# Optimization experiments

Hardware: AMD Instinct MI355X
Metric: run time of the kernel (lower is better)

Reference implementation:

```python
import jax, jax.numpy as jnp
import numpy as np

COEF_MEMORY = 0.2

def setup_inputs() -> dict:
    key = jax.random.key(0)
    k1, k2, k3, k4 = jax.random.split(key, 4)
    B, T, HW, C, Cv, M = 2, 8, 4096, 64, 3, 1024
    k = jax.random.normal(k1, (B, T, HW, C), dtype=jnp.float32)
    v = jax.random.normal(k2, (B, T, HW, Cv), dtype=jnp.float32)
    m_k = jax.random.normal(k3, (B, T - 1, M, C), dtype=jnp.float32)
    m_v = jax.random.normal(k4, (B, T - 1, M, Cv), dtype=jnp.float32)
    return {"k": k, "v": v, "m_k": m_k, "m_v": m_v}

def reference(k, v, m_k, m_v):
    # k: [B,T,HW,C] frame keys; v: [B,T,HW,Cv] frame values (quarter-res images)
    # m_k: [B,T-1,M,C] memory keys at step i; m_v: [B,T-1,M,Cv] memory values
    c = COEF_MEMORY
    k_i = k[:, :-1]  # ref keys  [B,T-1,HW,C]
    k_j = k[:, 1:]   # tar keys  [B,T-1,HW,C]
    v_i = v[:, :-1]  # ref vals  [B,T-1,HW,Cv]
    # frame-to-frame affinity: softmax over ref positions (last axis)
    sim_k = jax.nn.softmax(jnp.einsum('btqc,btkc->btqk', k_j, k_i), axis=-1)
    # memory-to-frame affinity: softmax over memory slots
    sim_m = jax.nn.softmax(jnp.einsum('btqc,btmc->btqm', k_j, m_k), axis=-1)
    rec_k = jnp.einsum('btqk,btkd->btqd', sim_k, v_i)   # [B,T-1,HW,Cv]
    rec_m = jnp.einsum('btqm,btmd->btqd', sim_m, m_v)   # [B,T-1,HW,Cv]
    return (1.0 - c) * rec_k + c * rec_m
```

## Files before the change

### kernel.cpp

```cpp
#include <hip/hip_runtime.h>

typedef __attribute__((ext_vector_type(2))) __fp16 h2;
typedef __attribute__((ext_vector_type(4))) __fp16 h4;
typedef __attribute__((ext_vector_type(8))) __fp16 h8;
typedef __attribute__((ext_vector_type(4))) float f32x4;

#define LOG2E 1.44269504088896340736f

__device__ __forceinline__ h2 pkrtz(float a, float b) {
    return __builtin_bit_cast(h2, __builtin_amdgcn_cvt_pkrtz(a, b));
}

__global__ __launch_bounds__(256) void kast_attn_kernel(
    const float* __restrict__ K,
    const float* __restrict__ V,
    const float* __restrict__ MK,
    const float* __restrict__ MV,
    float* __restrict__ OUT)
{
    __shared__ alignas(16) __fp16 sK[2][64][64];
    __shared__ alignas(16) __fp16 sVT[2][4][68];

    const int id = blockIdx.x;
    const int sw = (id & 7) * 112 + (id >> 3);
    const int bt = sw >> 6;
    const int qblk = sw & 63;
    const int b = bt / 7, t = bt % 7;

    const int tid = threadIdx.x;
    const int lane = tid & 63;
    const int w = tid >> 6;
    const int col = lane & 15;
    const int g = lane >> 4;

    const int r = tid >> 2;
    const int c0 = (tid & 3) * 16;
    const int rs = (r & 7) << 3;
    const unsigned vr = (unsigned)tid / 3u;
    const unsigned vd = (unsigned)tid - vr * 3u;

    if (tid < 128) sVT[tid >> 6][3][tid & 63] = (__fp16)1.0f;

    const float* Qbase = K + (((size_t)b * 8 + (t + 1)) * 4096) * 64;
    h8 aq[2];
    {
        const int qrow = qblk * 64 + w * 16 + col;
        const float* qp = Qbase + (size_t)qrow * 64;
#pragma unroll
        for (int ch = 0; ch < 2; ++ch) {
            const int cc = ch * 32 + g * 8;
            const f32x4 xa = *(const f32x4*)&qp[cc];
            const f32x4 xb = *(const f32x4*)&qp[cc + 4];
            const h2 p0 = pkrtz(xa[0] * LOG2E, xa[1] * LOG2E);
            const h2 p1 = pkrtz(xa[2] * LOG2E, xa[3] * LOG2E);
            const h2 p2 = pkrtz(xb[0] * LOG2E, xb[1] * LOG2E);
            const h2 p3 = pkrtz(xb[2] * LOG2E, xb[3] * LOG2E);
            aq[ch] = (h8){p0[0], p0[1], p1[0], p1[1], p2[0], p2[1], p3[0], p3[1]};
        }
    }

    float outc0 = 0.f, outc1 = 0.f, outc2 = 0.f;

    for (int phase = 0; phase < 2; ++phase) {
        const float* kp; const float* vp; int ntile; float wgt;
        if (phase == 0) {
            kp = K + (((size_t)b * 8 + t) * 4096) * 64;
            vp = V + (((size_t)b * 8 + t) * 4096) * 3;
            ntile = 64; wgt = 0.8f;
        } else {
            kp = MK + (((size_t)b * 7 + t) * 1024) * 64;
            vp = MV + (((size_t)b * 7 + t) * 1024) * 3;
            ntile = 16; wgt = 0.2f;
        }

        {
            const float* src = kp + ((size_t)r) * 64 + c0;
            const f32x4* s4 = (const f32x4*)src;
            const f32x4 ra = s4[0], rb = s4[1], rc = s4[2], rd = s4[3];
            const h2 q0 = pkrtz(ra[0], ra[1]), q1 = pkrtz(ra[2], ra[3]);
            const h2 q2 = pkrtz(rb[0], rb[1]), q3 = pkrtz(rb[2], rb[3]);
            const h2 q4 = pkrtz(rc[0], rc[1]), q5 = pkrtz(rc[2], rc[3]);
            const h2 q6 = pkrtz(rd[0], rd[1]), q7 = pkrtz(rd[2], rd[3]);
            *(h8*)&sK[0][r][c0 ^ rs] = (h8){q0[0], q0[1], q1[0], q1[1], q2[0], q2[1], q3[0], q3[1]};
            *(h8*)&sK[0][r][(c0 + 8) ^ rs] = (h8){q4[0], q4[1], q5[0], q5[1], q6[0], q6[1], q7[0], q7[1]};
            if (tid < 192) sVT[0][vd][vr] = (__fp16)vp[tid];
        }
        __syncthreads();

        float mrun = -1e30f;
        f32x4 O = (f32x4){0.f, 0.f, 0.f, 0.f};

        for (int kt = 0; kt < ntile; ++kt) {
            const int cur = kt & 1;
            const bool have = (kt + 1) < ntile;

            f32x4 ra, rb, rc, rd; float rv = 0.f;
            if (have) {
                const float* src = kp + ((size_t)(kt + 1) * 64 + r) * 64 + c0;
                const f32x4* s4 = (const f32x4*)src;
                ra = s4[0]; rb = s4[1]; rc = s4[2]; rd = s4[3];
                if (tid < 192) rv = vp[(size_t)(kt + 1) * 192 + tid];
            }

            f32x4 acc[4];
#pragma unroll
            for (int nt = 0; nt < 4; ++nt) acc[nt] = (f32x4){0.f, 0.f, 0.f, 0.f};
#pragma unroll
            for (int ch = 0; ch < 2; ++ch) {
                h8 bh[4];
#pragma unroll
                for (int nt = 0; nt < 4; ++nt) {
                    const int rr = nt * 16 + col;
                    const int cc = (ch * 32 + g * 8) ^ ((rr & 7) << 3);
                    bh[nt] = *(const h8*)&sK[cur][rr][cc];
                }
#pragma unroll
                for (int nt = 0; nt < 4; ++nt)
                    acc[nt] = __builtin_amdgcn_mfma_f32_16x16x32_f16(bh[nt], aq[ch], acc[nt], 0, 0, 0);
            }

            {
                float tm = acc[0][0];
#pragma unroll
                for (int nt = 0; nt < 4; ++nt)
#pragma unroll
                    for (int j = 0; j < 4; ++j) tm = fmaxf(tm, acc[nt][j]);
                tm = fmaxf(tm, __shfl_xor(tm, 16));
                tm = fmaxf(tm, __shfl_xor(tm, 32));

                if (!__all(tm <= mrun)) {
                    const float mnew = fmaxf(mrun, tm);
                    const float sc = __builtin_amdgcn_exp2f(mrun - mnew);
                    O *= sc;
                    mrun = mnew;
                }
            }

#pragma unroll
            for (int nt = 0; nt < 4; ++nt) {
                const float p0 = __builtin_amdgcn_exp2f(acc[nt][0] - mrun);
                const float p1 = __builtin_amdgcn_exp2f(acc[nt][1] - mrun);
                const float p2 = __builtin_amdgcn_exp2f(acc[nt][2] - mrun);
                const float p3 = __builtin_amdgcn_exp2f(acc[nt][3] - mrun);
                const h2 pa = pkrtz(p0, p1), pb = pkrtz(p2, p3);
                const h4 pf = (h4){pa[0], pa[1], pb[0], pb[1]};
                const h4 vf = *(const h4*)&sVT[cur][col & 3][nt * 16 + 4 * g];
                O = __builtin_amdgcn_mfma_f32_16x16x16f16(vf, pf, O, 0, 0, 0);
            }

            if (have) {
                const int nb = cur ^ 1;
                const h2 q0 = pkrtz(ra[0], ra[1]), q1 = pkrtz(ra[2], ra[3]);
                const h2 q2 = pkrtz(rb[0], rb[1]), q3 = pkrtz(rb[2], rb[3]);
                const h2 q4 = pkrtz(rc[0], rc[1]), q5 = pkrtz(rc[2], rc[3]);
                const h2 q6 = pkrtz(rd[0], rd[1]), q7 = pkrtz(rd[2], rd[3]);
                *(h8*)&sK[nb][r][c0 ^ rs] = (h8){q0[0], q0[1], q1[0], q1[1], q2[0], q2[1], q3[0], q3[1]};
                *(h8*)&sK[nb][r][(c0 + 8) ^ rs] = (h8){q4[0], q4[1], q5[0], q5[1], q6[0], q6[1], q7[0], q7[1]};
                if (tid < 192) sVT[nb][vd][vr] = (__fp16)rv;
            }
            __syncthreads();
        }

        const float inv = wgt / O[3];
        outc0 += O[0] * inv;
        outc1 += O[1] * inv;
        outc2 += O[2] * inv;
    }

    if (g == 0) {
        const int q = qblk * 64 + w * 16 + col;
        float* op = OUT + (((size_t)b * 7 + t) * 4096 + (size_t)q) * 3;
        op[0] = outc0; op[1] = outc1; op[2] = outc2;
    }
}

extern "C" void kernel_launch(void* const* d_in, const int* in_sizes, int n_in,
                              void* d_out, int out_size, void* d_ws, size_t ws_size,
                              hipStream_t stream) {
    const float* K  = (const float*)d_in[0];
    const float* V  = (const float*)d_in[1];
    const float* MK = (const float*)d_in[2];
    const float* MV = (const float*)d_in[3];
    float* OUT = (float*)d_out;
    dim3 grid(896);
    dim3 block(256);
    hipLaunchKernelGGL(kast_attn_kernel, grid, block, 0, stream, K, V, MK, MV, OUT);
}
```

Measured before the change: 119.6 us.

## Pre-convert K/V tiles to swizzled fp16 workspace and stream via global_load_lds

```diff
diff --git a/kernel.cpp b/kernel.cpp
--- a/kernel.cpp
+++ b/kernel.cpp
@@ -7,15 +7,214 @@
 
 #define LOG2E 1.44269504088896340736f
 
+#define WS_K    0ull
+#define WS_MK   7340032ull
+#define WS_VT   9175040ull
+#define WS_MVT  9633792ull
+#define WS_NEED 9748480ull
+
 __device__ __forceinline__ h2 pkrtz(float a, float b) {
     return __builtin_bit_cast(h2, __builtin_amdgcn_cvt_pkrtz(a, b));
 }
 
+__device__ __forceinline__ void gll16(const void* g, void* l) {
+    __builtin_amdgcn_global_load_lds(
+        (const __attribute__((address_space(1))) unsigned int*)g,
+        (__attribute__((address_space(3))) unsigned int*)l, 16, 0, 0);
+}
+
+__global__ __launch_bounds__(256) void kast_pre_kernel(
+    const float* __restrict__ K, const float* __restrict__ V,
+    const float* __restrict__ MK, const float* __restrict__ MV,
+    char* __restrict__ ws)
+{
+    const int id = blockIdx.x * 256 + threadIdx.x;
+    if (id < 573440) {
+        const bool ismk = id >= 458752;
+        const int lid = ismk ? id - 458752 : id;
+        const int c = lid & 7;
+        const int r = (lid >> 3) & 63;
+        int kt, s;
+        if (ismk) { kt = (lid >> 9) & 15; s = lid >> 13; }
+        else      { kt = (lid >> 9) & 63; s = lid >> 15; }
+        const int b = s / 7, t = s - b * 7;
+        const float* src = ismk
+            ? MK + (((size_t)(b * 7 + t) * 1024 + kt * 64 + r) * 64 + c * 8)
+            : K  + (((size_t)(b * 8 + t) * 4096 + kt * 64 + r) * 64 + c * 8);
+        const f32x4 xa = *(const f32x4*)src;
+        const f32x4 xb = *(const f32x4*)(src + 4);
+        const h2 q0 = pkrtz(xa[0], xa[1]), q1 = pkrtz(xa[2], xa[3]);
+        const h2 q2 = pkrtz(xb[0], xb[1]), q3 = pkrtz(xb[2], xb[3]);
+        const h8 out = {q0[0], q0[1], q1[0], q1[1], q2[0], q2[1], q3[0], q3[1]};
+        __fp16* dst = (__fp16*)(ws + (ismk ? WS_MK : WS_K))
+                    + (size_t)(ismk ? (s * 16 + kt) : (s * 64 + kt)) * 4096
+                    + r * 64 + ((c ^ (r & 7)) * 8);
+        *(h8*)dst = out;
+    } else {
+        const int vid = id - 573440;
+        const bool ismv = vid >= 57344;
+        const int lid = ismv ? vid - 57344 : vid;
+        const int c = lid & 15;
+        const int d = (lid >> 4) & 3;
+        int kt, s;
+        if (ismv) { kt = (lid >> 6) & 15; s = lid >> 10; }
+        else      { kt = (lid >> 6) & 63; s = lid >> 12; }
+        const int b = s / 7, t = s - b * 7;
+        const float* src = ismv
+            ? MV + (((size_t)(b * 7 + t) * 1024 + kt * 64 + c * 4) * 3)
+            : V  + (((size_t)(b * 8 + t) * 4096 + kt * 64 + c * 4) * 3);
+        float f0, f1, f2, f3;
+        if (d == 3) { f0 = f1 = f2 = f3 = 1.0f; }
+        else { f0 = src[d]; f1 = src[3 + d]; f2 = src[6 + d]; f3 = src[9 + d]; }
+        const h2 pa = pkrtz(f0, f1), pb = pkrtz(f2, f3);
+        const h4 out4 = {pa[0], pa[1], pb[0], pb[1]};
+        __fp16* dst = (__fp16*)(ws + (ismv ? WS_MVT : WS_VT))
+                    + (size_t)(ismv ? (s * 16 + kt) : (s * 64 + kt)) * 256
+                    + d * 64 + (4 * ((c >> 2) ^ d) + (c & 3)) * 4;
+        *(h4*)dst = out4;
+    }
+}
+
 __global__ __launch_bounds__(256) void kast_attn_kernel(
     const float* __restrict__ K,
-    const float* __restrict__ V,
-    const float* __restrict__ MK,
-    const float* __restrict__ MV,
+    const char* __restrict__ ws,
+    float* __restrict__ OUT)
+{
+    __shared__ alignas(16) __fp16 sK2[2][64][64];
+    __shared__ alignas(16) __fp16 sVT2[2][4][64];
+
+    const int id = blockIdx.x;
+    const int sw = (id & 7) * 112 + (id >> 3);
+    const int bt = sw >> 6;
+    const int qblk = sw & 63;
+    const int b = bt / 7, t = bt - b * 7;
+
+    const int tid = threadIdx.x;
+    const int lane = tid & 63;
+    const int w = tid >> 6;
+    const int col = lane & 15;
+    const int g = lane >> 4;
+    const int cs = col & 7;
+    const int d3 = col & 3;
+
+    const float* qp = K + (((size_t)b * 8 + (t + 1)) * 4096 + (size_t)(qblk * 64 + w * 16 + col)) * 64;
+    h8 aq[2];
+#pragma unroll
+    for (int ch = 0; ch < 2; ++ch) {
+        const int cc = ch * 32 + g * 8;
+        const f32x4 xa = *(const f32x4*)&qp[cc];
+        const f32x4 xb = *(const f32x4*)&qp[cc + 4];
+        const h2 p0 = pkrtz(xa[0] * LOG2E, xa[1] * LOG2E);
+        const h2 p1 = pkrtz(xa[2] * LOG2E, xa[3] * LOG2E);
+        const h2 p2 = pkrtz(xb[0] * LOG2E, xb[1] * LOG2E);
+        const h2 p3 = pkrtz(xb[2] * LOG2E, xb[3] * LOG2E);
+        aq[ch] = (h8){p0[0], p0[1], p1[0], p1[1], p2[0], p2[1], p3[0], p3[1]};
+    }
+
+    float outc0 = 0.f, outc1 = 0.f, outc2 = 0.f;
+
+    auto stageK = [&](const char* kb, int tkt, int buf) {
+        const char* ksrc = kb + (size_t)tkt * 8192 + w * 2048 + lane * 16;
+        char* kdst = ((char*)&sK2[buf][0][0]) + w * 2048 + lane * 16;
+        gll16(ksrc, kdst);
+        gll16(ksrc + 1024, kdst + 1024);
+    };
+
+    for (int phase = 0; phase < 2; ++phase) {
+        const char* kbase; const char* vbase; int ntile; float wgt;
+        if (phase == 0) {
+            kbase = ws + WS_K  + (size_t)bt * 64 * 8192;
+            vbase = ws + WS_VT + (size_t)bt * 64 * 512;
+            ntile = 64; wgt = 0.8f;
+        } else {
+            kbase = ws + WS_MK  + (size_t)bt * 16 * 8192;
+            vbase = ws + WS_MVT + (size_t)bt * 16 * 512;
+            ntile = 16; wgt = 0.2f;
+        }
+
+        stageK(kbase, 0, 0);
+        if (tid < 32)
+            ((f32x4*)&sVT2[0][0][0])[tid] = ((const f32x4*)vbase)[tid];
+        __syncthreads();
+
+        float mrun = -1e30f;
+        f32x4 O = (f32x4){0.f, 0.f, 0.f, 0.f};
+
+        for (int kt = 0; kt < ntile; ++kt) {
+            const int cur = kt & 1;
+            const int nb = cur ^ 1;
+
+            if (kt + 1 < ntile) {
+                stageK(kbase, kt + 1, nb);
+                if (tid < 32)
+                    ((f32x4*)&sVT2[nb][0][0])[tid] =
+                        ((const f32x4*)(vbase + (size_t)(kt + 1) * 512))[tid];
+            }
+
+            f32x4 acc[4];
+#pragma unroll
+            for (int nt = 0; nt < 4; ++nt) acc[nt] = (f32x4){0.f, 0.f, 0.f, 0.f};
+            __builtin_amdgcn_s_setprio(1);
+#pragma unroll
+            for (int ch = 0; ch < 2; ++ch) {
+                h8 bh[4];
+#pragma unroll
+                for (int nt = 0; nt < 4; ++nt)
+                    bh[nt] = *(const h8*)&sK2[cur][nt * 16 + col][((ch * 4 + g) ^ cs) * 8];
+#pragma unroll
+                for (int nt = 0; nt < 4; ++nt)
+                    acc[nt] = __builtin_amdgcn_mfma_f32_16x16x32_f16(bh[nt], aq[ch], acc[nt], 0, 0, 0);
+            }
+            __builtin_amdgcn_s_setprio(0);
+
+            {
+                float tm = acc[0][0];
+#pragma unroll
+                for (int nt = 0; nt < 4; ++nt)
+#pragma unroll
+                    for (int j = 0; j < 4; ++j) tm = fmaxf(tm, acc[nt][j]);
+                tm = fmaxf(tm, __shfl_xor(tm, 16));
+                tm = fmaxf(tm, __shfl_xor(tm, 32));
+                if (!__all(tm <= mrun)) {
+                    const float mnew = fmaxf(mrun, tm);
+                    const float sc = __builtin_amdgcn_exp2f(mrun - mnew);
+                    O *= sc;
+                    mrun = mnew;
+                }
+            }
+
+            const char* vtb = (const char*)&sVT2[cur][0][0] + d3 * 128;
+#pragma unroll
+            for (int nt = 0; nt < 4; ++nt) {
+                const float p0 = __builtin_amdgcn_exp2f(acc[nt][0] - mrun);
+                const float p1 = __builtin_amdgcn_exp2f(acc[nt][1] - mrun);
+                const float p2 = __builtin_amdgcn_exp2f(acc[nt][2] - mrun);
+                const float p3 = __builtin_amdgcn_exp2f(acc[nt][3] - mrun);
+                const h2 pa = pkrtz(p0, p1), pb = pkrtz(p2, p3);
+                const h4 pf = (h4){pa[0], pa[1], pb[0], pb[1]};
+                const h4 vf = *(const h4*)(vtb + (4 * (nt ^ d3) + g) * 8);
+                O = __builtin_amdgcn_mfma_f32_16x16x16f16(vf, pf, O, 0, 0, 0);
+            }
+
+            __syncthreads();
+        }
+
+        const float inv = wgt / O[3];
+        outc0 += O[0] * inv;
+        outc1 += O[1] * inv;
+        outc2 += O[2] * inv;
+    }
+
+    if (g == 0) {
+        const int q = qblk * 64 + w * 16 + col;
+        float* op = OUT + (((size_t)b * 7 + t) * 4096 + (size_t)q) * 3;
+        op[0] = outc0; op[1] = outc1; op[2] = outc2;
+    }
+}
+
+__global__ __launch_bounds__(256) void kast_attn_fb(
+    const float* __restrict__ K, const float* __restrict__ V,
+    const float* __restrict__ MK, const float* __restrict__ MV,
     float* __restrict__ OUT)
 {
     __shared__ alignas(16) __fp16 sK[2][64][64];
@@ -72,7 +271,6 @@
             vp = MV + (((size_t)b * 7 + t) * 1024) * 3;
             ntile = 16; wgt = 0.2f;
         }
-
         {
             const float* src = kp + ((size_t)r) * 64 + c0;
             const f32x4* s4 = (const f32x4*)src;
@@ -93,7 +291,6 @@
         for (int kt = 0; kt < ntile; ++kt) {
             const int cur = kt & 1;
             const bool have = (kt + 1) < ntile;
-
             f32x4 ra, rb, rc, rd; float rv = 0.f;
             if (have) {
                 const float* src = kp + ((size_t)(kt + 1) * 64 + r) * 64 + c0;
@@ -101,7 +298,6 @@
                 ra = s4[0]; rb = s4[1]; rc = s4[2]; rd = s4[3];
                 if (tid < 192) rv = vp[(size_t)(kt + 1) * 192 + tid];
             }
-
             f32x4 acc[4];
 #pragma unroll
             for (int nt = 0; nt < 4; ++nt) acc[nt] = (f32x4){0.f, 0.f, 0.f, 0.f};
@@ -118,7 +314,6 @@
                 for (int nt = 0; nt < 4; ++nt)
                     acc[nt] = __builtin_amdgcn_mfma_f32_16x16x32_f16(bh[nt], aq[ch], acc[nt], 0, 0, 0);
             }
-
             {
                 float tm = acc[0][0];
 #pragma unroll
@@ -127,7 +322,6 @@
                     for (int j = 0; j < 4; ++j) tm = fmaxf(tm, acc[nt][j]);
                 tm = fmaxf(tm, __shfl_xor(tm, 16));
                 tm = fmaxf(tm, __shfl_xor(tm, 32));
-
                 if (!__all(tm <= mrun)) {
                     const float mnew = fmaxf(mrun, tm);
                     const float sc = __builtin_amdgcn_exp2f(mrun - mnew);
@@ -135,7 +329,6 @@
                     mrun = mnew;
                 }
             }
-
 #pragma unroll
             for (int nt = 0; nt < 4; ++nt) {
                 const float p0 = __builtin_amdgcn_exp2f(acc[nt][0] - mrun);
@@ -147,7 +340,6 @@
                 const h4 vf = *(const h4*)&sVT[cur][col & 3][nt * 16 + 4 * g];
                 O = __builtin_amdgcn_mfma_f32_16x16x16f16(vf, pf, O, 0, 0, 0);
             }
-
             if (have) {
                 const int nb = cur ^ 1;
                 const h2 q0 = pkrtz(ra[0], ra[1]), q1 = pkrtz(ra[2], ra[3]);
@@ -160,7 +352,6 @@
             }
             __syncthreads();
         }
-
         const float inv = wgt / O[3];
         outc0 += O[0] * inv;
         outc1 += O[1] * inv;
@@ -182,7 +373,13 @@
     const float* MK = (const float*)d_in[2];
     const float* MV = (const float*)d_in[3];
     float* OUT = (float*)d_out;
-    dim3 grid(896);
-    dim3 block(256);
-    hipLaunchKernelGGL(kast_attn_kernel, grid, block, 0, stream, K, V, MK, MV, OUT);
-}
+    if (ws_size >= WS_NEED) {
+        hipLaunchKernelGGL(kast_pre_kernel, dim3(2520), dim3(256), 0, stream,
+                           K, V, MK, MV, (char*)d_ws);
+        hipLaunchKernelGGL(kast_attn_kernel, dim3(896), dim3(256), 0, stream,
+                           K, (const char*)d_ws, OUT);
+    } else {
+        hipLaunchKernelGGL(kast_attn_fb, dim3(896), dim3(256), 0, stream,
+                           K, V, MK, MV, OUT);
+    }
+}
```

Result: no change. 119.0 us (-0.5%).
